# Kernel tuning notes

Measured on AMD Instinct MI355X. Metric: run time of the kernel, lower is better.

Reference implementation:

```python
import jax, jax.numpy as jnp
import numpy as np

N = 100000        # nodes
E = 1600000       # edges
D = 32            # hidden dim
C = 2             # num classes
NL = 4            # layer_num - 1 GIN layers
G = 512           # graphs in batch
BN_EPS = 1e-3     # keras BatchNormalization default epsilon


def setup_inputs() -> dict:
    key = jax.random.key(0)
    ks = jax.random.split(key, 16)
    s = 0.1
    return {
        "node_embeddings": jax.random.normal(ks[0], (N, D), dtype=jnp.float32),
        "edge_index": jax.random.randint(ks[1], (2, E), 0, N, dtype=jnp.int32),
        "batch": jnp.sort(jax.random.randint(ks[2], (N,), 0, G, dtype=jnp.int32)),
        # MLP inner dense + BN (per GIN layer)
        "W1": jax.random.normal(ks[3], (NL, D, D), dtype=jnp.float32) * s,
        "b1": jnp.zeros((NL, D), jnp.float32),
        "bn1_g": jnp.ones((NL, D), jnp.float32),
        "bn1_b": jnp.zeros((NL, D), jnp.float32),
        # MLP output dense
        "W2": jax.random.normal(ks[4], (NL, D, D), dtype=jnp.float32) * s,
        "b2": jnp.zeros((NL, D), jnp.float32),
        # ApplyNodeFunc BN
        "bn2_g": jnp.ones((NL, D), jnp.float32),
        "bn2_b": jnp.zeros((NL, D), jnp.float32),
        # outer per-layer BN
        "norm_g": jnp.ones((NL, D), jnp.float32),
        "norm_b": jnp.zeros((NL, D), jnp.float32),
        # readout heads: one Dense(num_classes) per hidden_rep level (layer_num of them)
        "dense_W": jax.random.normal(ks[5], (NL + 1, D, C), dtype=jnp.float32) * s,
        "dense_b": jnp.zeros((NL + 1, C), jnp.float32),
    }


def _bn(x, g, b):
    # inference-mode BatchNorm with init moving stats (mean=0, var=1)
    return x * (g / jnp.sqrt(1.0 + BN_EPS)) + b


def reference(node_embeddings, edge_index, batch, W1, b1, bn1_g, bn1_b,
              W2, b2, bn2_g, bn2_b, norm_g, norm_b, dense_W, dense_b):
    src, dst = edge_index[0], edge_index[1]
    h = node_embeddings
    hidden = [h]
    for i in range(NL):
        # GIN aggregation: (1+eps)*h + sum of neighbor features (eps=0)
        agg = jax.ops.segment_sum(h[src], dst, num_segments=N)  # [N, D]
        z = h + agg
        # ApplyNodeFunc: MLP (Dense->BN->ReLU->Dense) then BN + ReLU
        z = jax.nn.relu(_bn(z @ W1[i] + b1[i], bn1_g[i], bn1_b[i]))
        z = z @ W2[i] + b2[i]
        z = jax.nn.relu(_bn(z, bn2_g[i], bn2_b[i]))
        # outer norm + relu
        h = jax.nn.relu(_bn(z, norm_g[i], norm_b[i]))
        hidden.append(h)
    # readout: segment-sum pooling per hidden level, Dense(num_classes), summed
    score = jnp.zeros((G, C), dtype=node_embeddings.dtype)
    for i, hr in enumerate(hidden):
        pool = jax.ops.segment_sum(hr, batch, num_segments=G)  # [G, D]
        score = score + pool @ dense_W[i] + dense_b[i]
    return jax.nn.softmax(score, axis=-1)
```

## Files before the change

### kernel.cpp

```cpp
#include <hip/hip_runtime.h>
#include <hip/hip_fp16.h>

#define NN 100000
#define EE 1600000
#define DD 32
#define CC 2
#define NLAYERS 4
#define GG 512

#define BSH 9
#define BW 512
#define NBUK ((NN + BW - 1) / BW)
#define CAP 12288
#define CH 2048
#define NPART ((EE + CH - 1) / CH)

__global__ void part_kernel(const int* __restrict__ ei,
                            int* __restrict__ gcur,
                            unsigned* __restrict__ part) {
    __shared__ unsigned sorted[CH];
    __shared__ unsigned char sbkt[CH];
    __shared__ int cnt[NBUK], offs[NBUK], cur[NBUK], gbs[NBUK];

    const int tid = threadIdx.x;
    const int eb  = blockIdx.x * CH;
    const int nch = min(CH, EE - eb);

    for (int b = tid; b < NBUK; b += 256) cnt[b] = 0;
    __syncthreads();
    for (int i = tid; i < nch; i += 256) {
        int dn = ei[EE + eb + i];
        atomicAdd(&cnt[dn >> BSH], 1);
    }
    __syncthreads();
    if (tid == 0) {
        int o = 0;
        for (int b = 0; b < NBUK; ++b) { offs[b] = o; o += cnt[b]; }
    }
    __syncthreads();
    if (tid < NBUK) {
        cur[tid] = offs[tid];
        gbs[tid] = cnt[tid] ? atomicAdd(&gcur[tid], cnt[tid]) : 0;
    }
    __syncthreads();
    for (int i = tid; i < nch; i += 256) {
        int s  = ei[eb + i];
        int dn = ei[EE + eb + i];
        int b  = dn >> BSH;
        unsigned pk = ((unsigned)(dn & (BW - 1)) << 17) | (unsigned)s;
        int p = atomicAdd(&cur[b], 1);
        sorted[p] = pk;
        sbkt[p]   = (unsigned char)b;
    }
    __syncthreads();
    for (int i = tid; i < nch; i += 256) {
        int b = sbkt[i];
        part[(size_t)b * CAP + gbs[b] + (i - offs[b])] = sorted[i];
    }
}

__global__ void bscan_kernel(const int* __restrict__ gcur,
                             int* __restrict__ bbase,
                             int* __restrict__ row_ptr) {
    if (threadIdx.x == 0 && blockIdx.x == 0) {
        int o = 0;
        for (int b = 0; b < NBUK; ++b) { bbase[b] = o; o += gcur[b]; }
        row_ptr[NN] = EE;
    }
}

__global__ void lcsr_kernel(const unsigned* __restrict__ part,
                            const int* __restrict__ gcur,
                            const int* __restrict__ bbase,
                            int* __restrict__ row_ptr,
                            int* __restrict__ csr_src) {
    __shared__ int hcnt[BW];
    __shared__ int a[2][BW];
    __shared__ int ccur[BW];
    const int t    = threadIdx.x;
    const int b    = blockIdx.x;
    const int cntb = gcur[b];
    const int base = bbase[b];
    const size_t pb = (size_t)b * CAP;

    hcnt[t] = 0;
    __syncthreads();
    for (int i = t; i < cntb; i += BW)
        atomicAdd(&hcnt[part[pb + i] >> 17], 1);
    __syncthreads();
    int x = hcnt[t];
    a[0][t] = x;
    __syncthreads();
    int cb = 0;
    for (int off = 1; off < BW; off <<= 1) {
        int v = a[cb][t];
        if (t >= off) v += a[cb][t - off];
        a[cb ^ 1][t] = v;
        cb ^= 1;
        __syncthreads();
    }
    const int excl = a[cb][t] - x;
    const int node = b * BW + t;
    if (node < NN) row_ptr[node] = base + excl;
    ccur[t] = excl;
    __syncthreads();
    for (int i = t; i < cntb; i += BW) {
        unsigned pk = part[pb + i];
        int dl  = pk >> 17;
        int pos = base + atomicAdd(&ccur[dl], 1);
        csr_src[pos] = (int)(pk & 0x1FFFFu);
    }
}

__global__ void cvt_kernel(const float* __restrict__ in,
                           __half* __restrict__ out) {
    int i = blockIdx.x * blockDim.x + threadIdx.x;
    float4 v = reinterpret_cast<const float4*>(in)[i];
    __half2* o = reinterpret_cast<__half2*>(out) + 2 * (size_t)i;
    o[0] = __floats2half2_rn(v.x, v.y);
    o[1] = __floats2half2_rn(v.z, v.w);
}

__global__ __launch_bounds__(256) void layer_kernel(
    const __half* __restrict__ h_in, __half* __restrict__ h_out,
    const int* __restrict__ row_ptr, const int* __restrict__ csr_src,
    const int* __restrict__ batch,
    const float* __restrict__ W1, const float* __restrict__ b1,
    const float* __restrict__ g1, const float* __restrict__ bt1,
    const float* __restrict__ W2, const float* __restrict__ b2,
    const float* __restrict__ g2, const float* __restrict__ bt2,
    const float* __restrict__ ng, const float* __restrict__ nb,
    const float* __restrict__ dWl, float* __restrict__ score) {
    __shared__ float sp[8 * DD];
    __shared__ float sdW[DD * CC];
    __shared__ float ss[GG * CC];
    __shared__ float zA[64][DD];
    __shared__ float z2loc[8][DD];

    const int tid = threadIdx.x;
    const int j = tid >> 5;
    const int d = tid & 31;

    if (tid < DD) {
        sp[0 * DD + tid] = b1[tid];
        sp[1 * DD + tid] = g1[tid];
        sp[2 * DD + tid] = bt1[tid];
        sp[3 * DD + tid] = b2[tid];
        sp[4 * DD + tid] = g2[tid];
        sp[5 * DD + tid] = bt2[tid];
        sp[6 * DD + tid] = ng[tid];
        sp[7 * DD + tid] = nb[tid];
    }
    if (tid < DD * CC) sdW[tid] = dWl[tid];
    for (int i = tid; i < GG * CC; i += 256) ss[i] = 0.f;

    const float invs = 1.0f / sqrtf(1.001f);
    const int base = blockIdx.x * 64;

    for (int s = 0; s < 8; ++s) {
        const int local = j * 8 + s;
        const int n = base + local;
        if (n >= NN) break;
        float acc = __half2float(h_in[(size_t)n * DD + d]);
        int e = row_ptr[n];
        const int e1 = row_ptr[n + 1];
        for (; e + 16 <= e1; e += 16) {
            int ix[16];
            #pragma unroll
            for (int i = 0; i < 16; ++i)
                ix[i] = __builtin_nontemporal_load(&csr_src[e + i]);
            __half v[16];
            #pragma unroll
            for (int i = 0; i < 16; ++i) v[i] = h_in[(size_t)ix[i] * DD + d];
            float t0 = ((__half2float(v[0]) + __half2float(v[1])) +
                        (__half2float(v[2]) + __half2float(v[3]))) +
                       ((__half2float(v[4]) + __half2float(v[5])) +
                        (__half2float(v[6]) + __half2float(v[7])));
            float t1 = ((__half2float(v[8]) + __half2float(v[9])) +
                        (__half2float(v[10]) + __half2float(v[11]))) +
                       ((__half2float(v[12]) + __half2float(v[13])) +
                        (__half2float(v[14]) + __half2float(v[15])));
            acc += t0 + t1;
        }
        if (e + 8 <= e1) {
            int ix[8];
            #pragma unroll
            for (int i = 0; i < 8; ++i)
                ix[i] = __builtin_nontemporal_load(&csr_src[e + i]);
            __half v[8];
            #pragma unroll
            for (int i = 0; i < 8; ++i) v[i] = h_in[(size_t)ix[i] * DD + d];
            acc += ((__half2float(v[0]) + __half2float(v[1])) +
                    (__half2float(v[2]) + __half2float(v[3]))) +
                   ((__half2float(v[4]) + __half2float(v[5])) +
                    (__half2float(v[6]) + __half2float(v[7])));
            e += 8;
        }
        if (e + 4 <= e1) {
            int ix[4];
            #pragma unroll
            for (int i = 0; i < 4; ++i)
                ix[i] = __builtin_nontemporal_load(&csr_src[e + i]);
            __half v[4];
            #pragma unroll
            for (int i = 0; i < 4; ++i) v[i] = h_in[(size_t)ix[i] * DD + d];
            acc += (__half2float(v[0]) + __half2float(v[1])) +
                   (__half2float(v[2]) + __half2float(v[3]));
            e += 4;
        }
        for (; e < e1; ++e)
            acc += __half2float(h_in[(size_t)csr_src[e] * DD + d]);
        zA[local][d] = acc;
    }
    __syncthreads();

    for (int s = 0; s < 8; ++s) {
        const int local = j * 8 + s;
        const int n = base + local;
        if (n >= NN) break;

        float a1 = sp[0 * DD + d];
        #pragma unroll
        for (int kk = 0; kk < DD; kk += 4) {
            const float4 zv = *reinterpret_cast<const float4*>(&zA[local][kk]);
            a1 += zv.x * W1[(kk + 0) * DD + d] + zv.y * W1[(kk + 1) * DD + d] +
                  zv.z * W1[(kk + 2) * DD + d] + zv.w * W1[(kk + 3) * DD + d];
        }
        float v = fmaxf(a1 * (sp[1 * DD + d] * invs) + sp[2 * DD + d], 0.f);
        z2loc[j][d] = v;

        float a2 = sp[3 * DD + d];
        #pragma unroll
        for (int kk = 0; kk < DD; kk += 4) {
            const float4 zv = *reinterpret_cast<const float4*>(&z2loc[j][kk]);
            a2 += zv.x * W2[(kk + 0) * DD + d] + zv.y * W2[(kk + 1) * DD + d] +
                  zv.z * W2[(kk + 2) * DD + d] + zv.w * W2[(kk + 3) * DD + d];
        }
        float w = fmaxf(a2 * (sp[4 * DD + d] * invs) + sp[5 * DD + d], 0.f);
        w = fmaxf(w * (sp[6 * DD + d] * invs) + sp[7 * DD + d], 0.f);
        h_out[(size_t)n * DD + d] = __float2half_rn(w);

        float p0 = w * sdW[d * CC + 0];
        float p1 = w * sdW[d * CC + 1];
        #pragma unroll
        for (int off = 16; off > 0; off >>= 1) {
            p0 += __shfl_xor(p0, off, 32);
            p1 += __shfl_xor(p1, off, 32);
        }
        if (d == 0) {
            int g = batch[n];
            atomicAdd(&ss[g * CC + 0], p0);
            atomicAdd(&ss[g * CC + 1], p1);
        }
    }
    __syncthreads();

    for (int i = tid; i < GG * CC; i += 256) {
        float v = ss[i];
        if (v != 0.f) atomicAdd(&score[i], v);
    }
}

__global__ void pool_kernel(const float* __restrict__ h,
                            const int* __restrict__ batch,
                            const float* __restrict__ Wd,
                            float* __restrict__ score) {
    __shared__ float ss[GG * CC];
    __shared__ float sW[DD * CC];
    const int tid = threadIdx.x;
    for (int i = tid; i < GG * CC; i += 256) ss[i] = 0.f;
    if (tid < DD * CC) sW[tid] = Wd[tid];
    __syncthreads();

    const int d = tid & 31;
    const int grp = tid >> 5;
    const int n0 = blockIdx.x * 512;
    const int n1 = (n0 + 512 < NN) ? (n0 + 512) : NN;

    for (int n = n0 + grp; n < n1; n += 8) {
        float v = h[(size_t)n * DD + d];
        float p0 = v * sW[d * CC + 0];
        float p1 = v * sW[d * CC + 1];
        #pragma unroll
        for (int off = 16; off > 0; off >>= 1) {
            p0 += __shfl_xor(p0, off, 32);
            p1 += __shfl_xor(p1, off, 32);
        }
        if (d == 0) {
            int g = batch[n];
            atomicAdd(&ss[g * CC + 0], p0);
            atomicAdd(&ss[g * CC + 1], p1);
        }
    }
    __syncthreads();

    for (int i = tid; i < GG * CC; i += 256) {
        float v = ss[i];
        if (v != 0.f) atomicAdd(&score[i], v);
    }
}

__global__ void softmax_kernel(const float* __restrict__ score,
                               const float* __restrict__ db,
                               float* __restrict__ out) {
    int g = blockIdx.x * blockDim.x + threadIdx.x;
    if (g >= GG) return;
    float bs0 = 0.f, bs1 = 0.f;
    #pragma unroll
    for (int i = 0; i <= NLAYERS; ++i) {
        bs0 += db[i * CC + 0];
        bs1 += db[i * CC + 1];
    }
    float s0 = score[g * CC + 0] + bs0;
    float s1 = score[g * CC + 1] + bs1;
    float m = fmaxf(s0, s1);
    float e0 = expf(s0 - m), e1 = expf(s1 - m);
    float inv = 1.f / (e0 + e1);
    out[g * CC + 0] = e0 * inv;
    out[g * CC + 1] = e1 * inv;
}

extern "C" void kernel_launch(void* const* d_in, const int* in_sizes, int n_in,
                              void* d_out, int out_size, void* d_ws, size_t ws_size,
                              hipStream_t stream) {
    (void)in_sizes; (void)n_in; (void)out_size; (void)ws_size;

    const float* node_emb = (const float*)d_in[0];
    const int*   ei       = (const int*)d_in[1];
    const int*   batch    = (const int*)d_in[2];
    const float* W1       = (const float*)d_in[3];
    const float* b1       = (const float*)d_in[4];
    const float* g1       = (const float*)d_in[5];
    const float* bt1      = (const float*)d_in[6];
    const float* W2       = (const float*)d_in[7];
    const float* b2       = (const float*)d_in[8];
    const float* g2       = (const float*)d_in[9];
    const float* bt2      = (const float*)d_in[10];
    const float* ng       = (const float*)d_in[11];
    const float* nb       = (const float*)d_in[12];
    const float* dW       = (const float*)d_in[13];
    const float* db       = (const float*)d_in[14];
    float* out = (float*)d_out;

    __half* hA16   = (__half*)d_ws;
    __half* hB16   = hA16 + (size_t)NN * DD;
    __half* hC16   = hB16 + (size_t)NN * DD;
    unsigned* part = (unsigned*)hB16;
    float* score   = (float*)(hC16 + (size_t)NN * DD);
    int* row_ptr   = (int*)(score + GG * CC);
    int* csr_src   = row_ptr + NN + 2;
    int* gcur      = csr_src + EE;
    int* bbase     = gcur + 256;

    hipMemsetAsync(gcur, 0, 256 * sizeof(int), stream);
    hipMemsetAsync(score, 0, GG * CC * sizeof(float), stream);

    part_kernel<<<NPART, 256, 0, stream>>>(ei, gcur, part);
    bscan_kernel<<<1, 64, 0, stream>>>(gcur, bbase, row_ptr);
    lcsr_kernel<<<NBUK, BW, 0, stream>>>(part, gcur, bbase, row_ptr, csr_src);

    cvt_kernel<<<(NN * DD / 4 + 255) / 256, 256, 0, stream>>>(node_emb, hC16);

    pool_kernel<<<(NN + 511) / 512, 256, 0, stream>>>(node_emb, batch, dW, score);

    const int layerGrid = (NN + 63) / 64;
    const __half* cur_in = hC16;
    __half* bufs[2] = {hA16, hB16};
    for (int i = 0; i < NLAYERS; ++i) {
        __half* o = bufs[i & 1];
        layer_kernel<<<layerGrid, 256, 0, stream>>>(
            cur_in, o, row_ptr, csr_src, batch,
            W1 + (size_t)i * DD * DD, b1 + i * DD, g1 + i * DD, bt1 + i * DD,
            W2 + (size_t)i * DD * DD, b2 + i * DD, g2 + i * DD, bt2 + i * DD,
            ng + i * DD, nb + i * DD,
            dW + (size_t)(i + 1) * DD * CC, score);
        cur_in = o;
    }

    softmax_kernel<<<(GG + 255) / 256, 256, 0, stream>>>(score, db, out);
}
```

Before: 476.9 us.

## Gather neighbor rows with 8-byte vector loads and fuse fp16 conversion into pooling

The aggregation loop is restructured so each 64-lane wavefront handles one node: 8 lanes cover a 32-wide fp16 row with 8-byte loads, and 8 edges are processed in parallel. Partial sums are then combined with cross-lane shuffles. This replaces the old scheme of 32 lanes each doing 2-byte scalar gathers with deep unrolling, and is meant to raise memory efficiency per gathered row. Separately, the fp32-to-fp16 conversion is merged into the level-0 pooling kernel, saving one kernel launch and one pass over the embeddings. The trade-offs are predicated-off lanes on nodes with low degree, plus extra shuffle reductions for each node.

```diff
diff --git a/kernel.cpp b/kernel.cpp
--- a/kernel.cpp
+++ b/kernel.cpp
@@ -112,13 +112,45 @@
     }
 }
 
-__global__ void cvt_kernel(const float* __restrict__ in,
-                           __half* __restrict__ out) {
-    int i = blockIdx.x * blockDim.x + threadIdx.x;
-    float4 v = reinterpret_cast<const float4*>(in)[i];
-    __half2* o = reinterpret_cast<__half2*>(out) + 2 * (size_t)i;
-    o[0] = __floats2half2_rn(v.x, v.y);
-    o[1] = __floats2half2_rn(v.z, v.w);
+__global__ void pool_cvt_kernel(const float* __restrict__ h,
+                                const int* __restrict__ batch,
+                                const float* __restrict__ Wd,
+                                float* __restrict__ score,
+                                __half* __restrict__ h16) {
+    __shared__ float ss[GG * CC];
+    __shared__ float sW[DD * CC];
+    const int tid = threadIdx.x;
+    for (int i = tid; i < GG * CC; i += 256) ss[i] = 0.f;
+    if (tid < DD * CC) sW[tid] = Wd[tid];
+    __syncthreads();
+
+    const int d = tid & 31;
+    const int grp = tid >> 5;
+    const int n0 = blockIdx.x * 512;
+    const int n1 = (n0 + 512 < NN) ? (n0 + 512) : NN;
+
+    for (int n = n0 + grp; n < n1; n += 8) {
+        float v = h[(size_t)n * DD + d];
+        h16[(size_t)n * DD + d] = __float2half_rn(v);
+        float p0 = v * sW[d * CC + 0];
+        float p1 = v * sW[d * CC + 1];
+        #pragma unroll
+        for (int off = 16; off > 0; off >>= 1) {
+            p0 += __shfl_xor(p0, off, 32);
+            p1 += __shfl_xor(p1, off, 32);
+        }
+        if (d == 0) {
+            int g = batch[n];
+            atomicAdd(&ss[g * CC + 0], p0);
+            atomicAdd(&ss[g * CC + 1], p1);
+        }
+    }
+    __syncthreads();
+
+    for (int i = tid; i < GG * CC; i += 256) {
+        float v = ss[i];
+        if (v != 0.f) atomicAdd(&score[i], v);
+    }
 }
 
 __global__ __launch_bounds__(256) void layer_kernel(
@@ -138,8 +170,6 @@
     __shared__ float z2loc[8][DD];
 
     const int tid = threadIdx.x;
-    const int j = tid >> 5;
-    const int d = tid & 31;
 
     if (tid < DD) {
         sp[0 * DD + tid] = b1[tid];
@@ -157,63 +187,56 @@
     const float invs = 1.0f / sqrtf(1.001f);
     const int base = blockIdx.x * 64;
 
-    for (int s = 0; s < 8; ++s) {
-        const int local = j * 8 + s;
-        const int n = base + local;
-        if (n >= NN) break;
-        float acc = __half2float(h_in[(size_t)n * DD + d]);
-        int e = row_ptr[n];
-        const int e1 = row_ptr[n + 1];
-        for (; e + 16 <= e1; e += 16) {
-            int ix[16];
+    {
+        const int wav = tid >> 6;
+        const int lid = tid & 63;
+        const int sub = lid >> 3;
+        const int sl  = lid & 7;
+
+        for (int s = 0; s < 16; ++s) {
+            const int local = wav * 16 + s;
+            const int n = base + local;
+            if (n >= NN) break;
+            const int e0 = row_ptr[n];
+            const int e1 = row_ptr[n + 1];
+            float a0 = 0.f, a1 = 0.f, a2 = 0.f, a3 = 0.f;
+            for (int t = e0; t < e1; t += 8) {
+                const int ee = t + sub;
+                const bool ok = ee < e1;
+                const int ix = csr_src[ok ? ee : (e1 - 1)];
+                const uint2 raw = *reinterpret_cast<const uint2*>(
+                    h_in + ((size_t)ix * DD + sl * 4));
+                const float2 f01 =
+                    __half22float2(*reinterpret_cast<const __half2*>(&raw.x));
+                const float2 f23 =
+                    __half22float2(*reinterpret_cast<const __half2*>(&raw.y));
+                if (ok) { a0 += f01.x; a1 += f01.y; a2 += f23.x; a3 += f23.y; }
+            }
             #pragma unroll
-            for (int i = 0; i < 16; ++i)
-                ix[i] = __builtin_nontemporal_load(&csr_src[e + i]);
-            __half v[16];
-            #pragma unroll
-            for (int i = 0; i < 16; ++i) v[i] = h_in[(size_t)ix[i] * DD + d];
-            float t0 = ((__half2float(v[0]) + __half2float(v[1])) +
-                        (__half2float(v[2]) + __half2float(v[3]))) +
-                       ((__half2float(v[4]) + __half2float(v[5])) +
-                        (__half2float(v[6]) + __half2float(v[7])));
-            float t1 = ((__half2float(v[8]) + __half2float(v[9])) +
-                        (__half2float(v[10]) + __half2float(v[11]))) +
-                       ((__half2float(v[12]) + __half2float(v[13])) +
-                        (__half2float(v[14]) + __half2float(v[15])));
-            acc += t0 + t1;
-        }
-        if (e + 8 <= e1) {
-            int ix[8];
-            #pragma unroll
-            for (int i = 0; i < 8; ++i)
-                ix[i] = __builtin_nontemporal_load(&csr_src[e + i]);
-            __half v[8];
-            #pragma unroll
-            for (int i = 0; i < 8; ++i) v[i] = h_in[(size_t)ix[i] * DD + d];
-            acc += ((__half2float(v[0]) + __half2float(v[1])) +
-                    (__half2float(v[2]) + __half2float(v[3]))) +
-                   ((__half2float(v[4]) + __half2float(v[5])) +
-                    (__half2float(v[6]) + __half2float(v[7])));
-            e += 8;
-        }
-        if (e + 4 <= e1) {
-            int ix[4];
-            #pragma unroll
-            for (int i = 0; i < 4; ++i)
-                ix[i] = __builtin_nontemporal_load(&csr_src[e + i]);
-            __half v[4];
-            #pragma unroll
-            for (int i = 0; i < 4; ++i) v[i] = h_in[(size_t)ix[i] * DD + d];
-            acc += (__half2float(v[0]) + __half2float(v[1])) +
-                   (__half2float(v[2]) + __half2float(v[3]));
-            e += 4;
-        }
-        for (; e < e1; ++e)
-            acc += __half2float(h_in[(size_t)csr_src[e] * DD + d]);
-        zA[local][d] = acc;
-    }
-    __syncthreads();
-
+            for (int off = 8; off < 64; off <<= 1) {
+                a0 += __shfl_xor(a0, off, 64);
+                a1 += __shfl_xor(a1, off, 64);
+                a2 += __shfl_xor(a2, off, 64);
+                a3 += __shfl_xor(a3, off, 64);
+            }
+            if (lid < 8) {
+                const uint2 sraw = *reinterpret_cast<const uint2*>(
+                    h_in + ((size_t)n * DD + sl * 4));
+                const float2 s01 =
+                    __half22float2(*reinterpret_cast<const __half2*>(&sraw.x));
+                const float2 s23 =
+                    __half22float2(*reinterpret_cast<const __half2*>(&sraw.y));
+                float4 r;
+                r.x = a0 + s01.x; r.y = a1 + s01.y;
+                r.z = a2 + s23.x; r.w = a3 + s23.y;
+                *reinterpret_cast<float4*>(&zA[local][sl * 4]) = r;
+            }
+        }
+    }
+    __syncthreads();
+
+    const int j = tid >> 5;
+    const int d = tid & 31;
     for (int s = 0; s < 8; ++s) {
         const int local = j * 8 + s;
         const int n = base + local;
@@ -242,45 +265,6 @@
 
         float p0 = w * sdW[d * CC + 0];
         float p1 = w * sdW[d * CC + 1];
-        #pragma unroll
-        for (int off = 16; off > 0; off >>= 1) {
-            p0 += __shfl_xor(p0, off, 32);
-            p1 += __shfl_xor(p1, off, 32);
-        }
-        if (d == 0) {
-            int g = batch[n];
-            atomicAdd(&ss[g * CC + 0], p0);
-            atomicAdd(&ss[g * CC + 1], p1);
-        }
-    }
-    __syncthreads();
-
-    for (int i = tid; i < GG * CC; i += 256) {
-        float v = ss[i];
-        if (v != 0.f) atomicAdd(&score[i], v);
-    }
-}
-
-__global__ void pool_kernel(const float* __restrict__ h,
-                            const int* __restrict__ batch,
-                            const float* __restrict__ Wd,
-                            float* __restrict__ score) {
-    __shared__ float ss[GG * CC];
-    __shared__ float sW[DD * CC];
-    const int tid = threadIdx.x;
-    for (int i = tid; i < GG * CC; i += 256) ss[i] = 0.f;
-    if (tid < DD * CC) sW[tid] = Wd[tid];
-    __syncthreads();
-
-    const int d = tid & 31;
-    const int grp = tid >> 5;
-    const int n0 = blockIdx.x * 512;
-    const int n1 = (n0 + 512 < NN) ? (n0 + 512) : NN;
-
-    for (int n = n0 + grp; n < n1; n += 8) {
-        float v = h[(size_t)n * DD + d];
-        float p0 = v * sW[d * CC + 0];
-        float p1 = v * sW[d * CC + 1];
         #pragma unroll
         for (int off = 16; off > 0; off >>= 1) {
             p0 += __shfl_xor(p0, off, 32);
@@ -349,7 +333,7 @@
     float* score   = (float*)(hC16 + (size_t)NN * DD);
     int* row_ptr   = (int*)(score + GG * CC);
     int* csr_src   = row_ptr + NN + 2;
-    int* gcur      = csr_src + EE;
+    int* gcur      = csr_src + EE + 16;
     int* bbase     = gcur + 256;
 
     hipMemsetAsync(gcur, 0, 256 * sizeof(int), stream);
@@ -359,9 +343,8 @@
     bscan_kernel<<<1, 64, 0, stream>>>(gcur, bbase, row_ptr);
     lcsr_kernel<<<NBUK, BW, 0, stream>>>(part, gcur, bbase, row_ptr, csr_src);
 
-    cvt_kernel<<<(NN * DD / 4 + 255) / 256, 256, 0, stream>>>(node_emb, hC16);
-
-    pool_kernel<<<(NN + 511) / 512, 256, 0, stream>>>(node_emb, batch, dW, score);
+    pool_cvt_kernel<<<(NN + 511) / 512, 256, 0, stream>>>(
+        node_emb, batch, dW, score, hC16);
 
     const int layerGrid = (NN + 63) / 64;
     const __half* cur_in = hC16;
```

Result: slower. 519.3 us (+8.9%).
